# Optimization experiments

Hardware: AMD Instinct MI355X
Metric: run time of the kernel (lower is better)

Reference implementation:

```python
import jax, jax.numpy as jnp
import numpy as np
from jax import lax

# Solver hyper-params for the smoothed robust-OT LP (fixed-iteration, jit-safe)
N_STEPS = 60
TAU = 0.05    # softmax temperature smoothing max over classes
RHO = 10.0    # quadratic penalty weight on the Wasserstein-cost constraint
LR = 0.5


def setup_inputs() -> dict:
    key = jax.random.key(0)
    ks = jax.random.split(key, 6)
    X = jax.random.normal(ks[0], (16, 96, 3, 64, 64), jnp.float32)
    Qr = jax.random.uniform(ks[1], (16, 10, 96), jnp.float32) + 0.1
    Q = Qr / Qr.sum(-1, keepdims=True)  # each (b,k) row is a distribution over samples
    conv_w = jax.random.normal(ks[2], (32, 3, 3, 3), jnp.float32) * 0.05
    conv_b = jnp.zeros((32,), jnp.float32)
    fc_w = jax.random.normal(ks[3], (256, 30752), jnp.float32) * 0.01
    fc_b = jnp.zeros((256,), jnp.float32)
    theta = jnp.ones((10,), jnp.float32) * 0.1
    return {"X": X, "Q": Q, "conv_w": conv_w, "conv_b": conv_b,
            "fc_w": fc_w, "fc_b": fc_b, "theta": theta}


def _features(X, conv_w, conv_b, fc_w, fc_b):
    B, S = X.shape[:2]
    x = X.reshape(B * S, *X.shape[2:])  # [B*S, C, H, W]
    x = lax.conv_general_dilated(x, conv_w, window_strides=(1, 1), padding='VALID',
                                 dimension_numbers=('NCHW', 'OIHW', 'NCHW'))
    x = jax.nn.relu(x + conv_b[None, :, None, None])
    x = lax.reduce_window(x, -jnp.inf, lax.max, (1, 1, 2, 2), (1, 1, 2, 2), 'VALID')
    # dropout is identity in eval mode
    x = x.reshape(B * S, -1)
    x = jax.nn.relu(x @ fc_w.T + fc_b)
    return x.reshape(B, S, -1)  # [B, S, F]


def _pairwise_sqdist(feats):
    n2 = (feats ** 2).sum(-1)  # [B, S]
    D = n2[:, :, None] + n2[:, None, :] - 2.0 * jnp.einsum('bif,bjf->bij', feats, feats)
    diag = jnp.diagonal(D, axis1=1, axis2=2)  # [B, S]
    return jnp.clip(D - diag[:, None, :], 0.0)


def _robust_ot_solve(D, Q, theta):
    # Approximate the CvxpyLayer LP:
    #   min_gamma sum_l max_k p_k[l]  s.t. gamma_k rows sum to Q_k, <gamma_k, C> <= theta_k
    # via mirror-descent on a row-stochastic parameterization (rows of gamma_k are
    # Q_k[i]-scaled softmaxes), with a smoothed max (logsumexp) and quadratic penalty.
    B, K, S = Q.shape

    def obj(A):
        gamma = Q[..., None] * jax.nn.softmax(A, axis=-1)      # [B,K,S,S]
        p = gamma.sum(axis=2)                                   # column sums [B,K,S]
        smooth_max = TAU * jax.nn.logsumexp(p / TAU, axis=1)    # [B,S]
        cost = jnp.einsum('bkij,bij->bk', gamma, D)             # [B,K]
        pen = jnp.sum(jax.nn.relu(cost - theta[None, :]) ** 2)
        return smooth_max.sum() + RHO * pen

    grad_obj = jax.grad(obj)

    @jax.checkpoint
    def step(A, _):
        return A - LR * grad_obj(A), None

    A0 = jnp.zeros((B, K, S, S), D.dtype)
    A, _ = lax.scan(step, A0, None, length=N_STEPS)
    gamma = Q[..., None] * jax.nn.softmax(A, axis=-1)
    return gamma.sum(axis=2)  # p_hat [B,K,S]


def reference(X, Q, conv_w, conv_b, fc_w, fc_b, theta):
    feats = _features(X, conv_w, conv_b, fc_w, fc_b)   # [B,S,F]
    D = _pairwise_sqdist(feats)                        # [B,S,S]
    p_hat = _robust_ot_solve(D, Q, theta)              # [B,K,S]
    return p_hat
```

## Files before the change

kernel.cpp:

```cpp
#include <hip/hip_runtime.h>

#define BB 16
#define SS 96
#define KK 10
#define FF 256
#define IH 64
#define IW 64
#define OCH 32
#define PH 31
#define PW 31
#define NPOS 961
#define FDIM 30752
#define NIMG 1536

#define TAUI 20.0f
#define RHOC 10.0f
#define LRC  0.5f
#define NSTEPS 60

#define KSPLIT 31
#define KCHE 992

typedef _Float16 v8hf __attribute__((ext_vector_type(8)));
typedef _Float16 v4hf __attribute__((ext_vector_type(4)));
typedef __fp16 h2 __attribute__((ext_vector_type(2)));
typedef float v4f __attribute__((ext_vector_type(4)));

__global__ __launch_bounds__(256)
void wcast(const float* __restrict__ w, _Float16* __restrict__ wh,
           const float* __restrict__ convw, __fp16* __restrict__ wpp) {
    const int t = blockIdx.x * 256 + threadIdx.x;
    if (t < 288) {
        const float* s = convw + t * 3;
        const __fp16 w0 = (__fp16)s[0], w1 = (__fp16)s[1], w2 = (__fp16)s[2];
        __fp16* d = wpp + t * 8;
        d[0] = w0; d[1] = w1;
        d[2] = w2; d[3] = (__fp16)0.f;
        d[4] = (__fp16)0.f; d[5] = w0;
        d[6] = w1; d[7] = w2;
    }
    const size_t i = ((size_t)blockIdx.x * 256 + threadIdx.x) * 4;
    float4 v = *(const float4*)(w + i);
    v4hf o = {(_Float16)v.x, (_Float16)v.y, (_Float16)v.z, (_Float16)v.w};
    *(v4hf*)(wh + i) = o;
}

__global__ __launch_bounds__(256)
void conv_pool(const float* __restrict__ X, const uint4* __restrict__ wp,
               const float* __restrict__ bias, _Float16* __restrict__ pooled) {
    __shared__ uint4 wsl[288];
    const int tid = threadIdx.x;
    for (int i = tid; i < 288; i += 256) wsl[i] = wp[i];
    __syncthreads();

    const int img = blockIdx.y;
    const int pos = blockIdx.x * 256 + tid;
    if (pos >= NPOS) return;
    const int oy = pos / PW, ox = pos % PW;
    const int iy = 2 * oy, ix = 2 * ox;
    const float* xb = X + (size_t)img * 3 * IH * IW;
    h2 inh[3][4][2];
#pragma unroll
    for (int c = 0; c < 3; c++)
#pragma unroll
        for (int r = 0; r < 4; r++) {
            const float* row = xb + ((size_t)c * IH + iy + r) * IW + ix;
            float2 p0 = *(const float2*)(row);
            float2 p1 = *(const float2*)(row + 2);
            inh[c][r][0] = __builtin_amdgcn_cvt_pkrtz(p0.x, p0.y);
            inh[c][r][1] = __builtin_amdgcn_cvt_pkrtz(p1.x, p1.y);
        }
    _Float16* outp = pooled + (size_t)img * FDIM + pos;
    for (int oc = 0; oc < OCH; oc++) {
        float a00 = 0.f, a01 = 0.f, a10 = 0.f, a11 = 0.f;
#pragma unroll
        for (int c = 0; c < 3; c++)
#pragma unroll
            for (int ky = 0; ky < 3; ky++) {
                const h2* q = (const h2*)(wsl + oc * 9 + c * 3 + ky);
                a00 = __builtin_amdgcn_fdot2(inh[c][ky][0], q[0], a00, false);
                a00 = __builtin_amdgcn_fdot2(inh[c][ky][1], q[1], a00, false);
                a01 = __builtin_amdgcn_fdot2(inh[c][ky][0], q[2], a01, false);
                a01 = __builtin_amdgcn_fdot2(inh[c][ky][1], q[3], a01, false);
                a10 = __builtin_amdgcn_fdot2(inh[c][ky + 1][0], q[0], a10, false);
                a10 = __builtin_amdgcn_fdot2(inh[c][ky + 1][1], q[1], a10, false);
                a11 = __builtin_amdgcn_fdot2(inh[c][ky + 1][0], q[2], a11, false);
                a11 = __builtin_amdgcn_fdot2(inh[c][ky + 1][1], q[3], a11, false);
            }
        float m = fmaxf(fmaxf(a00, a01), fmaxf(a10, a11)) + bias[oc];
        outp[(size_t)oc * NPOS] = (_Float16)fmaxf(m, 0.f);
    }
}

__global__ __launch_bounds__(256)
void fc_gemm(const _Float16* __restrict__ Ah, const _Float16* __restrict__ Wh,
             float* __restrict__ fpart) {
    __shared__ _Float16 Asl[128 * 56];
    __shared__ _Float16 Bsl[128 * 56];
    const int m0 = blockIdx.x * 128, n0 = blockIdx.y * 128;
    const int k0 = blockIdx.z * KCHE;
    const int tid = threadIdx.x;
    const int wave = tid >> 6, lane = tid & 63;
    const int quad = lane >> 4, l16 = lane & 15;
    const int wm = (wave & 1) * 64, wn = (wave >> 1) * 64;
    const int ar = tid >> 1, ac = (tid & 1) * 16;
    const _Float16* Ag = Ah + (size_t)(m0 + ar) * FDIM + ac;
    const _Float16* Bg = Wh + (size_t)(n0 + ar) * FDIM + ac;

    v4f acc[4][4];
#pragma unroll
    for (int i = 0; i < 4; i++)
#pragma unroll
        for (int j = 0; j < 4; j++) acc[i][j] = (v4f)(0.f);

    for (int s = 0; s < KCHE / 32; s++) {
        const int gk = k0 + (s << 5);
        uint4 a0 = *(const uint4*)(Ag + gk);
        uint4 a1 = *(const uint4*)(Ag + gk + 8);
        uint4 b0 = *(const uint4*)(Bg + gk);
        uint4 b1 = *(const uint4*)(Bg + gk + 8);
        __syncthreads();
        *(uint4*)&Asl[ar * 56 + ac] = a0;
        *(uint4*)&Asl[ar * 56 + ac + 8] = a1;
        *(uint4*)&Bsl[ar * 56 + ac] = b0;
        *(uint4*)&Bsl[ar * 56 + ac + 8] = b1;
        __syncthreads();
        v8hf af[4], bf[4];
#pragma unroll
        for (int mt = 0; mt < 4; mt++)
            af[mt] = *(const v8hf*)&Asl[(wm + mt * 16 + l16) * 56 + quad * 8];
#pragma unroll
        for (int nt = 0; nt < 4; nt++)
            bf[nt] = *(const v8hf*)&Bsl[(wn + nt * 16 + l16) * 56 + quad * 8];
#pragma unroll
        for (int mt = 0; mt < 4; mt++)
#pragma unroll
            for (int nt = 0; nt < 4; nt++)
                acc[mt][nt] = __builtin_amdgcn_mfma_f32_16x16x32_f16(
                    af[mt], bf[nt], acc[mt][nt], 0, 0, 0);
    }
    float* outz = fpart + (size_t)blockIdx.z * NIMG * FF;
#pragma unroll
    for (int mt = 0; mt < 4; mt++)
#pragma unroll
        for (int nt = 0; nt < 4; nt++)
#pragma unroll
            for (int i = 0; i < 4; i++) {
                const int gm = m0 + wm + mt * 16 + quad * 4 + i;
                const int gn = n0 + wn + nt * 16 + l16;
                outz[(size_t)gm * FF + gn] = acc[mt][nt][i];
            }
}

__global__ __launch_bounds__(256)
void bias_sum_relu(const float* __restrict__ fpart, const float* __restrict__ bias,
                   float* __restrict__ f, float* __restrict__ n2) {
    const int tid = threadIdx.x;
    const size_t idx = ((size_t)blockIdx.x * 256 + tid) * 4;
    float4 s = make_float4(0.f, 0.f, 0.f, 0.f);
#pragma unroll
    for (int z = 0; z < KSPLIT; z++) {
        float4 v = *(const float4*)(fpart + (size_t)z * NIMG * FF + idx);
        s.x += v.x; s.y += v.y; s.z += v.z; s.w += v.w;
    }
    const int col = (int)(idx & (FF - 1));
    float4 bv = *(const float4*)(bias + col);
    float4 o;
    o.x = fmaxf(s.x + bv.x, 0.f);
    o.y = fmaxf(s.y + bv.y, 0.f);
    o.z = fmaxf(s.z + bv.z, 0.f);
    o.w = fmaxf(s.w + bv.w, 0.f);
    *(float4*)(f + idx) = o;
    float sq = o.x * o.x + o.y * o.y + o.z * o.z + o.w * o.w;
#pragma unroll
    for (int mm = 32; mm >= 1; mm >>= 1) sq += __shfl_xor(sq, mm);
    if ((tid & 63) == 0) n2[blockIdx.x * 4 + (tid >> 6)] = sq;
}

__global__ __launch_bounds__(256)
void dmat(const float* __restrict__ feats, const float* __restrict__ n2,
          float* __restrict__ Dm) {
    const int i0 = blockIdx.x * 16, j0 = blockIdx.y * 16, b = blockIdx.z;
    __shared__ float fi[16][260], fj[16][260];
    const int tid = threadIdx.x;
    const int r = tid >> 4, c0 = (tid & 15) * 16;
    const float* fbase = feats + (size_t)b * SS * FF;
#pragma unroll
    for (int v = 0; v < 16; v += 4) {
        float4 a = *(const float4*)(fbase + (size_t)(i0 + r) * FF + c0 + v);
        float4 w = *(const float4*)(fbase + (size_t)(j0 + r) * FF + c0 + v);
        *(float4*)&fi[r][c0 + v] = a;
        *(float4*)&fj[r][c0 + v] = w;
    }
    __syncthreads();
    const int ti = tid >> 4, tj = tid & 15;
    float dot = 0.f;
#pragma unroll 4
    for (int f = 0; f < FF; f += 4) {
        float4 a = *(const float4*)&fi[ti][f];
        float4 w = *(const float4*)&fj[tj][f];
        dot += a.x * w.x + a.y * w.y + a.z * w.z + a.w * w.w;
    }
    const int i = i0 + ti, j = j0 + tj;
    const float d = n2[b * SS + i] + n2[b * SS + j] - 2.f * dot;
    Dm[((size_t)b * SS + i) * SS + j] = fmaxf(d, 0.f);
}

__global__ __launch_bounds__(512)
void ot_kernel(const float* __restrict__ Dg, const float* __restrict__ Qg,
               const float* __restrict__ thetag, float* __restrict__ ppub,
               unsigned* __restrict__ bar, float* __restrict__ out) {
    const int bk = blockIdx.x;
    const int b = bk / KK, k = bk % KK;
    const int tid = threadIdx.x;
    const int hw = tid >> 5, l = tid & 31;

    __shared__ float ppart[16][SS];
    __shared__ float cpart[16];
    __shared__ float Msh[SS];
    __shared__ float pown[SS];
    __shared__ float costsh, lamsh;

    float a[6][3], e[6][3], dre[6][3], rz[6], qi[6];

    const float* Db = Dg + (size_t)b * SS * SS;
    const float* Qb = Qg + ((size_t)b * KK + k) * SS;
#pragma unroll
    for (int r = 0; r < 6; r++) {
        const int i = hw * 6 + r;
#pragma unroll
        for (int u = 0; u < 3; u++) dre[r][u] = Db[i * SS + l + 32 * u];
        qi[r] = Qb[i];
    }
    const float th = thetag[k];
    unsigned* ctr = bar + b * 64;
    unsigned target = 0;

    auto publish_and_wait = [&](int buf) {
        if (tid < SS)
            __hip_atomic_store(&ppub[(((size_t)buf * BB + b) * KK + k) * SS + tid],
                               pown[tid], __ATOMIC_RELAXED, __HIP_MEMORY_SCOPE_AGENT);
        asm volatile("s_waitcnt vmcnt(0)" ::: "memory");
        __syncthreads();
        target += KK;
        if (tid == 0) {
            __hip_atomic_fetch_add(ctr, 1u, __ATOMIC_RELAXED, __HIP_MEMORY_SCOPE_AGENT);
            while (__hip_atomic_load(ctr, __ATOMIC_RELAXED, __HIP_MEMORY_SCOPE_AGENT) < target)
                __builtin_amdgcn_s_sleep(2);
        }
        __syncthreads();
    };

    auto collect = [&]() {
        __syncthreads();
        if (tid < SS) {
            float s = 0.f;
#pragma unroll
            for (int h = 0; h < 16; h++) s += ppart[h][tid];
            pown[tid] = s;
        }
        if (tid == 0) {
            float c = 0.f;
#pragma unroll
            for (int h = 0; h < 16; h++) c += cpart[h];
            costsh = c;
            lamsh = 2.f * RHOC * fmaxf(c - th, 0.f);
        }
        __syncthreads();
    };

    {
        float cd[6];
#pragma unroll
        for (int r = 0; r < 6; r++) {
#pragma unroll
            for (int u = 0; u < 3; u++) { a[r][u] = 0.f; e[r][u] = 1.f; }
            rz[r] = 1.f / 96.f;
            cd[r] = dre[r][0] + dre[r][1] + dre[r][2];
        }
#pragma unroll
        for (int mm = 16; mm >= 1; mm >>= 1)
#pragma unroll
            for (int r = 0; r < 6; r++) cd[r] += __shfl_xor(cd[r], mm);
        float pp0 = 0.f, cc = 0.f;
#pragma unroll
        for (int r = 0; r < 6; r++) {
            const float scale = qi[r] * rz[r];
            pp0 += scale;
            cc += scale * cd[r];
        }
        ppart[hw][l] = pp0; ppart[hw][l + 32] = pp0; ppart[hw][l + 64] = pp0;
        if (l == 0) cpart[hw] = cc;
        collect();
    }
    publish_and_wait(0);

    for (int t = 0; t < NSTEPS; t++) {
        const int rbuf = t & 1;
        if (tid < SS) {
            const float* ps = ppub + (((size_t)rbuf * BB + b) * KK) * SS + tid;
            float v[KK];
            float mx = -1e30f;
#pragma unroll
            for (int kk2 = 0; kk2 < KK; kk2++) {
                v[kk2] = __hip_atomic_load(&ps[kk2 * SS], __ATOMIC_RELAXED,
                                           __HIP_MEMORY_SCOPE_AGENT) * TAUI;
                mx = fmaxf(mx, v[kk2]);
            }
            float sum = 0.f;
#pragma unroll
            for (int kk2 = 0; kk2 < KK; kk2++) sum += __expf(v[kk2] - mx);
            Msh[tid] = __expf(v[k] - mx) * __builtin_amdgcn_rcpf(sum);
        }
        __syncthreads();
        const float lam = lamsh;
        const float M0 = Msh[l], M1 = Msh[l + 32], M2 = Msh[l + 64];

        float g[6][3], dt[6];
#pragma unroll
        for (int r = 0; r < 6; r++) {
            g[r][0] = fmaf(lam, dre[r][0], M0);
            g[r][1] = fmaf(lam, dre[r][1], M1);
            g[r][2] = fmaf(lam, dre[r][2], M2);
            dt[r] = (e[r][0] * g[r][0] + e[r][1] * g[r][1] + e[r][2] * g[r][2]) * rz[r];
        }
#pragma unroll
        for (int mm = 16; mm >= 1; mm >>= 1)
#pragma unroll
            for (int r = 0; r < 6; r++) dt[r] += __shfl_xor(dt[r], mm);

        float mrow[6];
#pragma unroll
        for (int r = 0; r < 6; r++) {
            const float cq = LRC * qi[r] * rz[r];
            a[r][0] -= cq * e[r][0] * (g[r][0] - dt[r]);
            a[r][1] -= cq * e[r][1] * (g[r][1] - dt[r]);
            a[r][2] -= cq * e[r][2] * (g[r][2] - dt[r]);
            mrow[r] = fmaxf(a[r][0], fmaxf(a[r][1], a[r][2]));
        }
#pragma unroll
        for (int mm = 16; mm >= 1; mm >>= 1)
#pragma unroll
            for (int r = 0; r < 6; r++) mrow[r] = fmaxf(mrow[r], __shfl_xor(mrow[r], mm));

        float zz[6], cd[6];
#pragma unroll
        for (int r = 0; r < 6; r++) {
            e[r][0] = __expf(a[r][0] - mrow[r]);
            e[r][1] = __expf(a[r][1] - mrow[r]);
            e[r][2] = __expf(a[r][2] - mrow[r]);
            zz[r] = e[r][0] + e[r][1] + e[r][2];
            cd[r] = e[r][0] * dre[r][0] + e[r][1] * dre[r][1] + e[r][2] * dre[r][2];
        }
#pragma unroll
        for (int mm = 16; mm >= 1; mm >>= 1)
#pragma unroll
            for (int r = 0; r < 6; r++) {
                zz[r] += __shfl_xor(zz[r], mm);
                cd[r] += __shfl_xor(cd[r], mm);
            }

        float pp0 = 0.f, pp1 = 0.f, pp2 = 0.f, cc = 0.f;
#pragma unroll
        for (int r = 0; r < 6; r++) {
            const float rzz = __builtin_amdgcn_rcpf(zz[r]);
            rz[r] = rzz;
            const float scale = qi[r] * rzz;
            pp0 += scale * e[r][0];
            pp1 += scale * e[r][1];
            pp2 += scale * e[r][2];
            cc += scale * cd[r];
        }
        ppart[hw][l] = pp0; ppart[hw][l + 32] = pp1; ppart[hw][l + 64] = pp2;
        if (l == 0) cpart[hw] = cc;
        collect();
        if (t < NSTEPS - 1) publish_and_wait((t + 1) & 1);
    }
    if (tid < SS) out[((size_t)b * KK + k) * SS + tid] = pown[tid];
}

extern "C" void kernel_launch(void* const* d_in, const int* in_sizes, int n_in,
                              void* d_out, int out_size, void* d_ws, size_t ws_size,
                              hipStream_t stream) {
    const float* X     = (const float*)d_in[0];
    const float* Q     = (const float*)d_in[1];
    const float* convw = (const float*)d_in[2];
    const float* convb = (const float*)d_in[3];
    const float* fcw   = (const float*)d_in[4];
    const float* fcb   = (const float*)d_in[5];
    const float* theta = (const float*)d_in[6];
    float* out = (float*)d_out;

    char* ws = (char*)d_ws;
    size_t off = 0;
    auto take = [&](size_t nbytes) {
        char* p = ws + off;
        off += (nbytes + 255) & ~(size_t)255;
        return (void*)p;
    };
    _Float16* pooled = (_Float16*)take((size_t)NIMG * FDIM * 2);
    _Float16* Wh     = (_Float16*)take((size_t)FF * FDIM * 2);
    float*    fpart  = (float*)take((size_t)KSPLIT * NIMG * FF * 4);
    float*    feats  = (float*)take((size_t)NIMG * FF * 4);
    float*    n2     = (float*)take((size_t)NIMG * 4);
    float*    Dm     = (float*)take((size_t)BB * SS * SS * 4);
    float*    ppub   = (float*)take((size_t)2 * BB * KK * SS * 4);
    __fp16*   wpp    = (__fp16*)take((size_t)288 * 8 * 2);
    unsigned* bar    = (unsigned*)take((size_t)BB * 64 * 4);

    (void)hipMemsetAsync(bar, 0, (size_t)BB * 64 * 4, stream);

    hipLaunchKernelGGL(wcast, dim3((FF * FDIM) / 1024), dim3(256), 0, stream,
                       fcw, Wh, convw, (__fp16*)wpp);
    hipLaunchKernelGGL(conv_pool, dim3(4, NIMG), dim3(256), 0, stream,
                       X, (const uint4*)wpp, convb, pooled);
    hipLaunchKernelGGL(fc_gemm, dim3(12, 2, KSPLIT), dim3(256), 0, stream, pooled, Wh, fpart);
    hipLaunchKernelGGL(bias_sum_relu, dim3(NIMG * FF / 1024), dim3(256), 0, stream,
                       fpart, fcb, feats, n2);
    hipLaunchKernelGGL(dmat, dim3(6, 6, BB), dim3(256), 0, stream, feats, n2, Dm);
    hipLaunchKernelGGL(ot_kernel, dim3(BB * KK), dim3(512), 0, stream, Dm, Q, theta, ppub, bar, out);
}
```

Baseline: 601.9 us.

## Fuse conv+pool with weight cast and compute conv via MFMA from LDS

The separate weight-cast and conv/pool kernels are merged into one launch. Each image block now stages its input in LDS as fp16 and computes the 3x3 conv as an implicit GEMM with 16x16x32 f16 MFMA instructions, padding K from 27 to 32. The 2x2 max-pool is done with a register max plus a lane shuffle. This replaces per-thread fdot2 loops and removes one launch, at the cost of about 25KB of LDS per block, im2col gathers from LDS and scattered fp16 stores.

Result: faster. 549.5 us (-8.7%).

```diff
diff --git a/kernel.cpp b/kernel.cpp
--- a/kernel.cpp
+++ b/kernel.cpp
@@ -21,74 +21,102 @@
 #define KSPLIT 31
 #define KCHE 992
 
+#define WCBLK ((FF * FDIM) / 1024)
+
 typedef _Float16 v8hf __attribute__((ext_vector_type(8)));
 typedef _Float16 v4hf __attribute__((ext_vector_type(4)));
 typedef __fp16 h2 __attribute__((ext_vector_type(2)));
 typedef float v4f __attribute__((ext_vector_type(4)));
 
 __global__ __launch_bounds__(256)
-void wcast(const float* __restrict__ w, _Float16* __restrict__ wh,
-           const float* __restrict__ convw, __fp16* __restrict__ wpp) {
-    const int t = blockIdx.x * 256 + threadIdx.x;
-    if (t < 288) {
-        const float* s = convw + t * 3;
-        const __fp16 w0 = (__fp16)s[0], w1 = (__fp16)s[1], w2 = (__fp16)s[2];
-        __fp16* d = wpp + t * 8;
-        d[0] = w0; d[1] = w1;
-        d[2] = w2; d[3] = (__fp16)0.f;
-        d[4] = (__fp16)0.f; d[5] = w0;
-        d[6] = w1; d[7] = w2;
-    }
-    const size_t i = ((size_t)blockIdx.x * 256 + threadIdx.x) * 4;
-    float4 v = *(const float4*)(w + i);
-    v4hf o = {(_Float16)v.x, (_Float16)v.y, (_Float16)v.z, (_Float16)v.w};
-    *(v4hf*)(wh + i) = o;
-}
-
-__global__ __launch_bounds__(256)
-void conv_pool(const float* __restrict__ X, const uint4* __restrict__ wp,
-               const float* __restrict__ bias, _Float16* __restrict__ pooled) {
-    __shared__ uint4 wsl[288];
+void prep(const float* __restrict__ X, const float* __restrict__ convw,
+          const float* __restrict__ bias, _Float16* __restrict__ pooled,
+          const float* __restrict__ fcw, _Float16* __restrict__ wh) {
     const int tid = threadIdx.x;
-    for (int i = tid; i < 288; i += 256) wsl[i] = wp[i];
+    if (blockIdx.x >= NIMG) {
+        const size_t i = ((size_t)(blockIdx.x - NIMG) * 256 + tid) * 4;
+        float4 v = *(const float4*)(fcw + i);
+        v4hf o = {(_Float16)v.x, (_Float16)v.y, (_Float16)v.z, (_Float16)v.w};
+        *(v4hf*)(wh + i) = o;
+        return;
+    }
+    __shared__ _Float16 Xl[3 * 64 * 64 + 256];
+    __shared__ _Float16 Wl[32 * 32];
+    const int img = blockIdx.x;
+    const float* xb = X + (size_t)img * (3 * IH * IW);
+#pragma unroll
+    for (int i = 0; i < 12; i++) {
+        const int e = tid + i * 256;
+        float4 v = *(const float4*)(xb + (size_t)e * 4);
+        h2 p0 = __builtin_amdgcn_cvt_pkrtz(v.x, v.y);
+        h2 p1 = __builtin_amdgcn_cvt_pkrtz(v.z, v.w);
+        *(h2*)&Xl[e * 4] = p0;
+        *(h2*)&Xl[e * 4 + 2] = p1;
+    }
+    for (int t = tid; t < 1024; t += 256) {
+        const int oc = t >> 5, k = t & 31;
+        Wl[t] = (k < 27) ? (_Float16)convw[oc * 27 + k] : (_Float16)0.f;
+    }
     __syncthreads();
 
-    const int img = blockIdx.y;
-    const int pos = blockIdx.x * 256 + tid;
-    if (pos >= NPOS) return;
-    const int oy = pos / PW, ox = pos % PW;
-    const int iy = 2 * oy, ix = 2 * ox;
-    const float* xb = X + (size_t)img * 3 * IH * IW;
-    h2 inh[3][4][2];
-#pragma unroll
-    for (int c = 0; c < 3; c++)
-#pragma unroll
-        for (int r = 0; r < 4; r++) {
-            const float* row = xb + ((size_t)c * IH + iy + r) * IW + ix;
-            float2 p0 = *(const float2*)(row);
-            float2 p1 = *(const float2*)(row + 2);
-            inh[c][r][0] = __builtin_amdgcn_cvt_pkrtz(p0.x, p0.y);
-            inh[c][r][1] = __builtin_amdgcn_cvt_pkrtz(p1.x, p1.y);
-        }
-    _Float16* outp = pooled + (size_t)img * FDIM + pos;
-    for (int oc = 0; oc < OCH; oc++) {
-        float a00 = 0.f, a01 = 0.f, a10 = 0.f, a11 = 0.f;
-#pragma unroll
-        for (int c = 0; c < 3; c++)
-#pragma unroll
-            for (int ky = 0; ky < 3; ky++) {
-                const h2* q = (const h2*)(wsl + oc * 9 + c * 3 + ky);
-                a00 = __builtin_amdgcn_fdot2(inh[c][ky][0], q[0], a00, false);
-                a00 = __builtin_amdgcn_fdot2(inh[c][ky][1], q[1], a00, false);
-                a01 = __builtin_amdgcn_fdot2(inh[c][ky][0], q[2], a01, false);
-                a01 = __builtin_amdgcn_fdot2(inh[c][ky][1], q[3], a01, false);
-                a10 = __builtin_amdgcn_fdot2(inh[c][ky + 1][0], q[0], a10, false);
-                a10 = __builtin_amdgcn_fdot2(inh[c][ky + 1][1], q[1], a10, false);
-                a11 = __builtin_amdgcn_fdot2(inh[c][ky + 1][0], q[2], a11, false);
-                a11 = __builtin_amdgcn_fdot2(inh[c][ky + 1][1], q[3], a11, false);
+    const int lane = tid & 63;
+    const int l16 = lane & 15, q = lane >> 4;
+    const int wv = tid >> 6;
+    v8hf a0 = *(const v8hf*)&Wl[l16 * 32 + q * 8];
+    v8hf a1 = *(const v8hf*)&Wl[(16 + l16) * 32 + q * 8];
+    int off[8];
+#pragma unroll
+    for (int j = 0; j < 8; j++) {
+        const int k = q * 8 + j;
+        const int c = k / 9, rem = k - c * 9;
+        const int ky = rem / 3, kx = rem - ky * 3;
+        off[j] = c * 4096 + ky * 64 + kx;
+    }
+    const bool hi_ok = (q < 3);
+    float b0r[4], b1r[4];
+#pragma unroll
+    for (int i = 0; i < 4; i++) {
+        b0r[i] = bias[q * 4 + i];
+        b1r[i] = bias[16 + q * 4 + i];
+    }
+    _Float16* outp = pooled + (size_t)img * FDIM;
+
+    for (int oy = wv; oy < PH; oy += 4) {
+        const int y0 = oy * 2;
+#pragma unroll
+        for (int xt = 0; xt < 4; xt++) {
+            const int x = xt * 16 + l16;
+            const int base0 = y0 * 64 + x;
+            v8hf bf0, bf1;
+#pragma unroll
+            for (int j = 0; j < 8; j++) {
+                _Float16 h0 = Xl[base0 + off[j]];
+                _Float16 h1 = Xl[base0 + 64 + off[j]];
+                if (j >= 3 && !hi_ok) { h0 = (_Float16)0.f; h1 = (_Float16)0.f; }
+                bf0[j] = h0; bf1[j] = h1;
             }
-        float m = fmaxf(fmaxf(a00, a01), fmaxf(a10, a11)) + bias[oc];
-        outp[(size_t)oc * NPOS] = (_Float16)fmaxf(m, 0.f);
+            v4f c00 = (v4f)(0.f), c10 = (v4f)(0.f), c01 = (v4f)(0.f), c11 = (v4f)(0.f);
+            c00 = __builtin_amdgcn_mfma_f32_16x16x32_f16(a0, bf0, c00, 0, 0, 0);
+            c10 = __builtin_amdgcn_mfma_f32_16x16x32_f16(a1, bf0, c10, 0, 0, 0);
+            c01 = __builtin_amdgcn_mfma_f32_16x16x32_f16(a0, bf1, c01, 0, 0, 0);
+            c11 = __builtin_amdgcn_mfma_f32_16x16x32_f16(a1, bf1, c11, 0, 0, 0);
+            const int ox = xt * 8 + (l16 >> 1);
+            const bool act = ((l16 & 1) == 0) && (ox < PW);
+#pragma unroll
+            for (int i = 0; i < 4; i++) {
+                float m0 = fmaxf(c00[i], c01[i]);
+                float m1 = fmaxf(c10[i], c11[i]);
+                m0 = fmaxf(m0, __shfl_xor(m0, 1));
+                m1 = fmaxf(m1, __shfl_xor(m1, 1));
+                if (act) {
+                    const int oc0 = q * 4 + i;
+                    const float r0 = fmaxf(m0 + b0r[i], 0.f);
+                    const float r1 = fmaxf(m1 + b1r[i], 0.f);
+                    outp[(size_t)oc0 * NPOS + oy * PW + ox] = (_Float16)r0;
+                    outp[(size_t)(16 + oc0) * NPOS + oy * PW + ox] = (_Float16)r1;
+                }
+            }
+        }
     }
 }
 
@@ -405,15 +433,12 @@
     float*    n2     = (float*)take((size_t)NIMG * 4);
     float*    Dm     = (float*)take((size_t)BB * SS * SS * 4);
     float*    ppub   = (float*)take((size_t)2 * BB * KK * SS * 4);
-    __fp16*   wpp    = (__fp16*)take((size_t)288 * 8 * 2);
     unsigned* bar    = (unsigned*)take((size_t)BB * 64 * 4);
 
     (void)hipMemsetAsync(bar, 0, (size_t)BB * 64 * 4, stream);
 
-    hipLaunchKernelGGL(wcast, dim3((FF * FDIM) / 1024), dim3(256), 0, stream,
-                       fcw, Wh, convw, (__fp16*)wpp);
-    hipLaunchKernelGGL(conv_pool, dim3(4, NIMG), dim3(256), 0, stream,
-                       X, (const uint4*)wpp, convb, pooled);
+    hipLaunchKernelGGL(prep, dim3(NIMG + WCBLK), dim3(256), 0, stream,
+                       X, convw, convb, pooled, fcw, Wh);
     hipLaunchKernelGGL(fc_gemm, dim3(12, 2, KSPLIT), dim3(256), 0, stream, pooled, Wh, fpart);
     hipLaunchKernelGGL(bias_sum_relu, dim3(NIMG * FF / 1024), dim3(256), 0, stream,
                        fpart, fcb, feats, n2);
```
